# Optimization experiments

Measured on AMD Instinct MI355X. Metric: run time of the kernel, lower is better.

Reference implementation:

```python
import jax, jax.numpy as jnp
import numpy as np

N, E = 50000, 1600000
FEAT, HID, HEADS = 256, 64, 2
NEG_SLOPE = 0.2


def gat_conv(x, src, dst, W, att_src, att_dst, bias, heads, out_ch):
    """PyG GATConv (concat=True, self-loops already appended to src/dst)."""
    n = x.shape[0]
    h = (x @ W).reshape(n, heads, out_ch)                      # [N,H,C]
    a_src = jnp.einsum('nhc,hc->nh', h, att_src)               # [N,H]
    a_dst = jnp.einsum('nhc,hc->nh', h, att_dst)               # [N,H]
    alpha = jax.nn.leaky_relu(a_src[src] + a_dst[dst], NEG_SLOPE)  # [E',H]
    # segment softmax over incoming edges of each dst node
    amax = jax.ops.segment_max(alpha, dst, num_segments=n)
    alpha = jnp.exp(alpha - amax[dst])
    denom = jax.ops.segment_sum(alpha, dst, num_segments=n)
    alpha = alpha / (denom[dst] + 1e-16)
    msg = h[src] * alpha[..., None]                            # [E',H,C]
    out = jax.ops.segment_sum(msg, dst, num_segments=n)        # [N,H,C]
    return out.reshape(n, heads * out_ch) + bias


def setup_inputs() -> dict:
    key = jax.random.key(0)
    ks = jax.random.split(key, 10)
    x = jax.random.normal(ks[0], (N, FEAT), dtype=jnp.float32)
    edge_index = jax.random.randint(ks[1], (2, E), 0, N, dtype=jnp.int64)
    s1 = 1.0 / np.sqrt(FEAT)
    s2 = 1.0 / np.sqrt(HID * HEADS)
    sa = 1.0 / np.sqrt(HID)
    return {
        'x': x,
        'edge_index': edge_index,
        'W1': jax.random.uniform(ks[2], (FEAT, HEADS * HID), jnp.float32, -s1, s1),
        'att_src1': jax.random.uniform(ks[3], (HEADS, HID), jnp.float32, -sa, sa),
        'att_dst1': jax.random.uniform(ks[4], (HEADS, HID), jnp.float32, -sa, sa),
        'b1': jnp.zeros((HEADS * HID,), jnp.float32),
        'W2': jax.random.uniform(ks[5], (HEADS * HID, HID), jnp.float32, -s2, s2),
        'att_src2': jax.random.uniform(ks[6], (1, HID), jnp.float32, -sa, sa),
        'att_dst2': jax.random.uniform(ks[7], (1, HID), jnp.float32, -sa, sa),
        'b2': jnp.zeros((HID,), jnp.float32),
    }


def reference(x, edge_index, W1, att_src1, att_dst1, b1, W2, att_src2, att_dst2, b2):
    n = x.shape[0]
    loop = jnp.arange(n, dtype=edge_index.dtype)
    src = jnp.concatenate([edge_index[0], loop])   # add self loops (PyG default)
    dst = jnp.concatenate([edge_index[1], loop])
    h = gat_conv(x, src, dst, W1, att_src1, att_dst1, b1, HEADS, HID)
    h = jax.nn.relu(h)  # dropout is identity in eval mode
    h = gat_conv(h, src, dst, W2, att_src2, att_dst2, b2, 1, HID)
    return jax.nn.log_softmax(h, axis=1)
```

## Files before the change

kernel.cpp:

```cpp
#include <hip/hip_runtime.h>
#include <hip/hip_bf16.h>
#include <math.h>

typedef short bf16x8 __attribute__((ext_vector_type(8)));
typedef float f32x4 __attribute__((ext_vector_type(4)));

#define BSHIFT 7
#define BWIDTH 128
#define PCHUNK 4096


__global__ void zero_buf(int* __restrict__ p, int n) {
    int i = blockIdx.x * blockDim.x + threadIdx.x;
    if (i < n) p[i] = 0;
}

__global__ __launch_bounds__(256) void bucket_hist(const int* __restrict__ ei, int E,
                                                   int* __restrict__ bcnt) {
    __shared__ int h[512];
    int tid = threadIdx.x;
    for (int i = tid; i < 512; i += 256) h[i] = 0;
    __syncthreads();
    int start = blockIdx.x * PCHUNK;
    int cnt = min(PCHUNK, E - start);
    for (int i = tid; i < cnt; i += 256)
        atomicAdd(&h[ei[E + start + i] >> BSHIFT], 1);
    __syncthreads();
    for (int i = tid; i < 512; i += 256)
        if (h[i]) atomicAdd(&bcnt[i], h[i]);
}

__global__ __launch_bounds__(512) void bucket_scan(const int* __restrict__ bcnt,
                                                   int* __restrict__ bbase,
                                                   int* __restrict__ bcur,
                                                   int nbk, int n) {
    __shared__ int s[512];
    int tid = threadIdx.x;
    int nodes = 0;
    if (tid < nbk) nodes = min(BWIDTH, n - (tid << BSHIFT));
    int v = (tid < nbk) ? bcnt[tid] + nodes : 0;
    s[tid] = v;
    __syncthreads();
    #pragma unroll
    for (int o = 1; o < 512; o <<= 1) {
        int t = (tid >= o) ? s[tid - o] : 0;
        __syncthreads();
        s[tid] += t;
        __syncthreads();
    }
    if (tid < nbk) {
        int ex = s[tid] - v;
        bbase[tid] = ex;
        bcur[tid] = ex - (tid << BSHIFT);
    }
    if (tid == nbk) bbase[nbk] = s[tid];
}

__global__ __launch_bounds__(256) void partition_edges(const int* __restrict__ ei, int E,
                                                       int* __restrict__ bcur,
                                                       int* __restrict__ tmp) {
    __shared__ int2 stage[PCHUNK];
    __shared__ int h[512];
    __shared__ int lbase[512];
    int tid = threadIdx.x;
    int start = blockIdx.x * PCHUNK;
    int cnt = min(PCHUNK, E - start);
    for (int i = tid; i < 512; i += 256) h[i] = 0;
    __syncthreads();
    for (int i = tid; i < cnt; i += 256) {
        int s = ei[start + i];
        int d = ei[E + start + i];
        stage[i] = make_int2(s, d);
        atomicAdd(&h[d >> BSHIFT], 1);
    }
    __syncthreads();
    for (int i = tid; i < 512; i += 256) {
        if (h[i] > 0) lbase[i] = atomicAdd(&bcur[i], h[i]);
        h[i] = 0;
    }
    __syncthreads();
    for (int i = tid; i < cnt; i += 256) {
        int2 e = stage[i];
        int b = e.y >> BSHIFT;
        int r = atomicAdd(&h[b], 1);
        tmp[lbase[b] + r] = (e.x << BSHIFT) | (e.y & (BWIDTH - 1));
    }
}

__global__ __launch_bounds__(256) void bucket_csr(const int* __restrict__ bbase,
                                                  const int* __restrict__ tmp,
                                                  int* __restrict__ offs,
                                                  int* __restrict__ srcs,
                                                  int n, int nbk) {
    __shared__ int cnt[BWIDTH];
    __shared__ int sa[BWIDTH];
    __shared__ int cur[BWIDTH];
    int b = blockIdx.x;
    int tid = threadIdx.x;
    int node0 = b << BSHIFT;
    int nnodes = min(BWIDTH, n - node0);
    int cb = bbase[b];
    int ce = bbase[b + 1];
    int tb = cb - node0;
    int ecnt = (ce - cb) - nnodes;

    if (tid < BWIDTH) cnt[tid] = (tid < nnodes) ? 1 : 0;
    __syncthreads();
    for (int i = tid; i < ecnt; i += 256)
        atomicAdd(&cnt[tmp[tb + i] & (BWIDTH - 1)], 1);
    __syncthreads();
    if (tid < BWIDTH) sa[tid] = cnt[tid];
    __syncthreads();
    #pragma unroll
    for (int o = 1; o < BWIDTH; o <<= 1) {
        int v = 0;
        if (tid < BWIDTH) { v = sa[tid]; if (tid >= o) v += sa[tid - o]; }
        __syncthreads();
        if (tid < BWIDTH) sa[tid] = v;
        __syncthreads();
    }
    if (tid < BWIDTH) {
        int ex = sa[tid] - cnt[tid];
        if (tid < nnodes) {
            offs[node0 + tid] = cb + ex;
            srcs[cb + ex] = node0 + tid;
        }
        cur[tid] = ex + (tid < nnodes ? 1 : 0);
    }
    if (b == nbk - 1 && tid == 0) offs[n] = ce;
    __syncthreads();
    for (int i = tid; i < ecnt; i += 256) {
        int e = tmp[tb + i];
        int li = e & (BWIDTH - 1);
        int r = atomicAdd(&cur[li], 1);
        srcs[cb + r] = e >> BSHIFT;
    }
}

__global__ void transpose_both(const float* __restrict__ W1, const float* __restrict__ W2,
                               __hip_bfloat16* __restrict__ W1t,
                               __hip_bfloat16* __restrict__ W2t) {
    int idx = blockIdx.x * blockDim.x + threadIdx.x;
    const int n1 = 128 * 256;
    if (idx < n1) {
        int nn = idx >> 8, kk = idx & 255;
        W1t[idx] = __float2bfloat16(W1[kk * 128 + nn]);
    } else {
        int j = idx - n1;
        if (j < 64 * 128) {
            int nn = j >> 7, kk = j & 127;
            W2t[j] = __float2bfloat16(W2[kk * 64 + nn]);
        }
    }
}

template <bool A_BF16, int NT, int HEADS>
__global__ __launch_bounds__(256) void gemm_att(
    const void* __restrict__ Av, const __hip_bfloat16* __restrict__ Bt,
    __hip_bfloat16* __restrict__ C,
    const float* __restrict__ atts, const float* __restrict__ attd,
    float* __restrict__ a_s, float* __restrict__ a_d, int M, int K) {
    constexpr int N = NT * 16;
    __shared__ __hip_bfloat16 As[64][40];
    int tid = threadIdx.x;
    int w = tid >> 6, l = tid & 63;
    int q = l >> 4, m16 = l & 15;
    int bm = blockIdx.x * 64;

    int lr = tid >> 2, lseg = tid & 3;
    int arow = bm + lr; if (arow >= M) arow = M - 1;

    f32x4 acc[NT];
    #pragma unroll
    for (int t = 0; t < NT; t++) acc[t] = (f32x4){0.f, 0.f, 0.f, 0.f};

    for (int kc = 0; kc < K; kc += 32) {
        if (A_BF16) {
            const __hip_bfloat16* A = (const __hip_bfloat16*)Av;
            uint4 v = *(const uint4*)(A + (size_t)arow * K + kc + lseg * 8);
            *(uint4*)&As[lr][lseg * 8] = v;
        } else {
            const float* A = (const float*)Av;
            float4 v0 = *(const float4*)(A + (size_t)arow * K + kc + lseg * 8);
            float4 v1 = *(const float4*)(A + (size_t)arow * K + kc + lseg * 8 + 4);
            union { __hip_bfloat16 h[8]; uint4 u; } tmp;
            tmp.h[0] = __float2bfloat16(v0.x); tmp.h[1] = __float2bfloat16(v0.y);
            tmp.h[2] = __float2bfloat16(v0.z); tmp.h[3] = __float2bfloat16(v0.w);
            tmp.h[4] = __float2bfloat16(v1.x); tmp.h[5] = __float2bfloat16(v1.y);
            tmp.h[6] = __float2bfloat16(v1.z); tmp.h[7] = __float2bfloat16(v1.w);
            *(uint4*)&As[lr][lseg * 8] = tmp.u;
        }
        __syncthreads();
        bf16x8 a = *(const bf16x8*)&As[w * 16 + m16][q * 8];
        #pragma unroll
        for (int t = 0; t < NT; t++) {
            bf16x8 b = *(const bf16x8*)(Bt + (size_t)(t * 16 + m16) * K + kc + q * 8);
            acc[t] = __builtin_amdgcn_mfma_f32_16x16x32_bf16(a, b, acc[t], 0, 0, 0);
        }
        __syncthreads();
    }

    #pragma unroll
    for (int t = 0; t < NT; t++) {
        #pragma unroll
        for (int r = 0; r < 4; r++) {
            int row = bm + w * 16 + q * 4 + r;
            if (row < M) C[(size_t)row * N + t * 16 + m16] = __float2bfloat16(acc[t][r]);
        }
    }

    float ps[HEADS][4], pd[HEADS][4];
    #pragma unroll
    for (int hh = 0; hh < HEADS; hh++)
        #pragma unroll
        for (int r = 0; r < 4; r++) { ps[hh][r] = 0.f; pd[hh][r] = 0.f; }
    #pragma unroll
    for (int t = 0; t < NT; t++) {
        int ch = t * 16 + m16;
        float asw = atts[ch], adw = attd[ch];
        int hh = (HEADS == 2) ? (t >> 2) : 0;
        #pragma unroll
        for (int r = 0; r < 4; r++) {
            ps[hh][r] = fmaf(acc[t][r], asw, ps[hh][r]);
            pd[hh][r] = fmaf(acc[t][r], adw, pd[hh][r]);
        }
    }
    #pragma unroll
    for (int o = 1; o < 16; o <<= 1) {
        #pragma unroll
        for (int hh = 0; hh < HEADS; hh++)
            #pragma unroll
            for (int r = 0; r < 4; r++) {
                ps[hh][r] += __shfl_xor(ps[hh][r], o);
                pd[hh][r] += __shfl_xor(pd[hh][r], o);
            }
    }
    if (m16 == 0) {
        #pragma unroll
        for (int r = 0; r < 4; r++) {
            int row = bm + w * 16 + q * 4 + r;
            if (row < M) {
                if (HEADS == 2) {
                    a_s[row * 2]     = ps[0][r];
                    a_s[row * 2 + 1] = ps[1][r];
                    a_d[row * 2]     = pd[0][r];
                    a_d[row * 2 + 1] = pd[1][r];
                } else {
                    a_s[row] = ps[0][r];
                    a_d[row] = pd[0][r];
                }
            }
        }
    }
}

__device__ __forceinline__ float leaky(float r) {
    return r < 0.f ? 0.2f * r : r;
}

__device__ __forceinline__ void unpack2(unsigned u, float& lo, float& hi) {
    lo = __uint_as_float(u << 16);
    hi = __uint_as_float(u & 0xffff0000u);
}

__global__ __launch_bounds__(256) void edge_agg_l1(
    const int* __restrict__ offs, const int* __restrict__ srcs,
    const __hip_bfloat16* __restrict__ h1, const float* __restrict__ asv,
    const float* __restrict__ adv, const float* __restrict__ bias,
    __hip_bfloat16* __restrict__ out, int n) {
    int wid = (blockIdx.x * blockDim.x + threadIdx.x) >> 6;
    int lane = threadIdx.x & 63;
    int d = wid >> 1;
    int h = wid & 1;
    if (d >= n) return;
    int start = offs[d], end = offs[d + 1];
    float adh = adv[2 * d + h];

    float m = -3.4e38f, ssum = 0.f;
    for (int e = start + lane; e < end; e += 64) {
        int s = srcs[e];
        float r = leaky(asv[2 * s + h] + adh);
        if (r > m) { ssum *= __expf(m - r); m = r; }
        ssum += __expf(r - m);
    }
    #pragma unroll
    for (int o = 1; o < 64; o <<= 1) {
        float om = __shfl_xor(m, o), os = __shfl_xor(ssum, o);
        float nm = fmaxf(m, om);
        ssum = ssum * __expf(m - nm) + os * __expf(om - nm);
        m = nm;
    }
    float inv = 1.f / (ssum + 1e-16f);

    int sub = lane & 7;
    int g = lane >> 3;
    int ch0 = h * 64 + sub * 8;

    float acc[8];
    #pragma unroll
    for (int k = 0; k < 8; k++) acc[k] = 0.f;

    for (int base = start; base < end; base += 64) {
        int cnt = min(64, end - base);
        int s_l = 0;
        float w_l = 0.f;
        if (lane < cnt) {
            s_l = srcs[base + lane];
            w_l = __expf(leaky(asv[2 * s_l + h] + adh) - m) * inv;
        }
        int steps = (cnt + 7) >> 3;
        for (int jj = 0; jj < steps; ++jj) {
            int e = jj * 8 + g;
            float we = __shfl(w_l, e);
            int se = __shfl(s_l, e);
            uint4 v = *(const uint4*)(h1 + (size_t)se * 128 + ch0);
            float f0, f1, f2, f3, f4, f5, f6, f7;
            unpack2(v.x, f0, f1);
            unpack2(v.y, f2, f3);
            unpack2(v.z, f4, f5);
            unpack2(v.w, f6, f7);
            acc[0] = fmaf(we, f0, acc[0]);
            acc[1] = fmaf(we, f1, acc[1]);
            acc[2] = fmaf(we, f2, acc[2]);
            acc[3] = fmaf(we, f3, acc[3]);
            acc[4] = fmaf(we, f4, acc[4]);
            acc[5] = fmaf(we, f5, acc[5]);
            acc[6] = fmaf(we, f6, acc[6]);
            acc[7] = fmaf(we, f7, acc[7]);
        }
    }
    #pragma unroll
    for (int o = 8; o < 64; o <<= 1)
        #pragma unroll
        for (int k = 0; k < 8; k++) acc[k] += __shfl_xor(acc[k], o);

    if (lane < 8) {
        float4 b0 = *(const float4*)(bias + ch0);
        float4 b1 = *(const float4*)(bias + ch0 + 4);
        union { __hip_bfloat16 h[8]; uint4 u; } o2;
        o2.h[0] = __float2bfloat16(fmaxf(acc[0] + b0.x, 0.f));
        o2.h[1] = __float2bfloat16(fmaxf(acc[1] + b0.y, 0.f));
        o2.h[2] = __float2bfloat16(fmaxf(acc[2] + b0.z, 0.f));
        o2.h[3] = __float2bfloat16(fmaxf(acc[3] + b0.w, 0.f));
        o2.h[4] = __float2bfloat16(fmaxf(acc[4] + b1.x, 0.f));
        o2.h[5] = __float2bfloat16(fmaxf(acc[5] + b1.y, 0.f));
        o2.h[6] = __float2bfloat16(fmaxf(acc[6] + b1.z, 0.f));
        o2.h[7] = __float2bfloat16(fmaxf(acc[7] + b1.w, 0.f));
        *(uint4*)(out + (size_t)d * 128 + ch0) = o2.u;
    }
}

__global__ __launch_bounds__(256) void edge_agg_l2(
    const int* __restrict__ offs, const int* __restrict__ srcs,
    const __hip_bfloat16* __restrict__ h2, const float* __restrict__ asv,
    const float* __restrict__ adv, const float* __restrict__ bias,
    float* __restrict__ out, int n) {
    int d = (blockIdx.x * blockDim.x + threadIdx.x) >> 6;
    int lane = threadIdx.x & 63;
    if (d >= n) return;
    int start = offs[d], end = offs[d + 1];
    float ad = adv[d];

    float m = -3.4e38f, ssum = 0.f;
    for (int e = start + lane; e < end; e += 64) {
        int s = srcs[e];
        float r = leaky(asv[s] + ad);
        if (r > m) { ssum *= __expf(m - r); m = r; }
        ssum += __expf(r - m);
    }
    #pragma unroll
    for (int o = 1; o < 64; o <<= 1) {
        float om = __shfl_xor(m, o), os = __shfl_xor(ssum, o);
        float nm = fmaxf(m, om);
        ssum = ssum * __expf(m - nm) + os * __expf(om - nm);
        m = nm;
    }
    float inv = 1.f / (ssum + 1e-16f);

    int sub = lane & 7;
    int g = lane >> 3;
    int ch0 = sub * 8;

    float acc[8];
    #pragma unroll
    for (int k = 0; k < 8; k++) acc[k] = 0.f;

    for (int base = start; base < end; base += 64) {
        int cnt = min(64, end - base);
        int s_l = 0;
        float w_l = 0.f;
        if (lane < cnt) {
            s_l = srcs[base + lane];
            w_l = __expf(leaky(asv[s_l] + ad) - m) * inv;
        }
        int steps = (cnt + 7) >> 3;
        for (int jj = 0; jj < steps; ++jj) {
            int e = jj * 8 + g;
            float we = __shfl(w_l, e);
            int se = __shfl(s_l, e);
            uint4 v = *(const uint4*)(h2 + (size_t)se * 64 + ch0);
            float f0, f1, f2, f3, f4, f5, f6, f7;
            unpack2(v.x, f0, f1);
            unpack2(v.y, f2, f3);
            unpack2(v.z, f4, f5);
            unpack2(v.w, f6, f7);
            acc[0] = fmaf(we, f0, acc[0]);
            acc[1] = fmaf(we, f1, acc[1]);
            acc[2] = fmaf(we, f2, acc[2]);
            acc[3] = fmaf(we, f3, acc[3]);
            acc[4] = fmaf(we, f4, acc[4]);
            acc[5] = fmaf(we, f5, acc[5]);
            acc[6] = fmaf(we, f6, acc[6]);
            acc[7] = fmaf(we, f7, acc[7]);
        }
    }
    #pragma unroll
    for (int o = 8; o < 64; o <<= 1)
        #pragma unroll
        for (int k = 0; k < 8; k++) acc[k] += __shfl_xor(acc[k], o);

    float4 b0 = *(const float4*)(bias + ch0);
    float4 b1 = *(const float4*)(bias + ch0 + 4);
    float v[8];
    v[0] = acc[0] + b0.x; v[1] = acc[1] + b0.y;
    v[2] = acc[2] + b0.z; v[3] = acc[3] + b0.w;
    v[4] = acc[4] + b1.x; v[5] = acc[5] + b1.y;
    v[6] = acc[6] + b1.z; v[7] = acc[7] + b1.w;

    float vm = v[0];
    #pragma unroll
    for (int k = 1; k < 8; k++) vm = fmaxf(vm, v[k]);
    #pragma unroll
    for (int o = 1; o < 8; o <<= 1) vm = fmaxf(vm, __shfl_xor(vm, o));
    float se_loc = 0.f;
    #pragma unroll
    for (int k = 0; k < 8; k++) se_loc += __expf(v[k] - vm);
    #pragma unroll
    for (int o = 1; o < 8; o <<= 1) se_loc += __shfl_xor(se_loc, o);
    float lse = vm + logf(se_loc);

    if (lane < 8) {
        float4 o0 = make_float4(v[0] - lse, v[1] - lse, v[2] - lse, v[3] - lse);
        float4 o1 = make_float4(v[4] - lse, v[5] - lse, v[6] - lse, v[7] - lse);
        *(float4*)(out + (size_t)d * 64 + ch0) = o0;
        *(float4*)(out + (size_t)d * 64 + ch0 + 4) = o1;
    }
}

extern "C" void kernel_launch(void* const* d_in, const int* in_sizes, int n_in,
                              void* d_out, int out_size, void* d_ws, size_t ws_size,
                              hipStream_t stream) {
    const float* x    = (const float*)d_in[0];
    const int*   ei   = (const int*)d_in[1];
    const float* W1   = (const float*)d_in[2];
    const float* as1w = (const float*)d_in[3];
    const float* ad1w = (const float*)d_in[4];
    const float* b1   = (const float*)d_in[5];
    const float* W2   = (const float*)d_in[6];
    const float* as2w = (const float*)d_in[7];
    const float* ad2w = (const float*)d_in[8];
    const float* b2   = (const float*)d_in[9];
    float* out = (float*)d_out;

    const int n = in_sizes[0] / 256;
    const int E = in_sizes[1] / 2;
    const int tot = E + n;
    const int nbk = (n + BWIDTH - 1) / BWIDTH;

    char* p = (char*)d_ws;
    auto alloc = [&](size_t bytes) {
        void* r = (void*)p;
        p += (bytes + 255) & ~(size_t)255;
        return r;
    };
    int*   offs  = (int*)alloc((size_t)(n + 1) * 4);
    int*   srcs  = (int*)alloc((size_t)tot * 4);
    int*   tmp   = (int*)alloc((size_t)E * 4);
    int*   bcnt  = (int*)alloc(512 * 4);
    int*   bbase = (int*)alloc(512 * 4);
    int*   bcur  = (int*)alloc(512 * 4);
    __hip_bfloat16* W1t = (__hip_bfloat16*)alloc((size_t)128 * 256 * 2);
    __hip_bfloat16* W2t = (__hip_bfloat16*)alloc((size_t)64 * 128 * 2);
    __hip_bfloat16* h1  = (__hip_bfloat16*)alloc((size_t)n * 128 * 2);
    __hip_bfloat16* out1= (__hip_bfloat16*)alloc((size_t)n * 128 * 2);
    __hip_bfloat16* h2  = (__hip_bfloat16*)alloc((size_t)n * 64 * 2);
    float* a_s1 = (float*)alloc((size_t)n * 2 * 4);
    float* a_d1 = (float*)alloc((size_t)n * 2 * 4);
    float* a_s2 = (float*)alloc((size_t)n * 4);
    float* a_d2 = (float*)alloc((size_t)n * 4);

    int pblocks = (E + PCHUNK - 1) / PCHUNK;

    zero_buf<<<2, 256, 0, stream>>>(bcnt, 512);
    bucket_hist<<<pblocks, 256, 0, stream>>>(ei, E, bcnt);
    bucket_scan<<<1, 512, 0, stream>>>(bcnt, bbase, bcur, nbk, n);
    partition_edges<<<pblocks, 256, 0, stream>>>(ei, E, bcur, tmp);
    bucket_csr<<<nbk, 256, 0, stream>>>(bbase, tmp, offs, srcs, n, nbk);

    transpose_both<<<(128 * 256 + 64 * 128 + 255) / 256, 256, 0, stream>>>(W1, W2, W1t, W2t);

    gemm_att<false, 8, 2><<<(n + 63) / 64, 256, 0, stream>>>(
        x, W1t, h1, as1w, ad1w, a_s1, a_d1, n, 256);
    edge_agg_l1<<<((size_t)n * 2 * 64 + 255) / 256, 256, 0, stream>>>(
        offs, srcs, h1, a_s1, a_d1, b1, out1, n);

    gemm_att<true, 4, 1><<<(n + 63) / 64, 256, 0, stream>>>(
        out1, W2t, h2, as2w, ad2w, a_s2, a_d2, n, 128);
    edge_agg_l2<<<((size_t)n * 64 + 255) / 256, 256, 0, stream>>>(
        offs, srcs, h2, a_s2, a_d2, b2, out, n);
}
```

Measured before the change: 319.4 us.

## Use single-pass online softmax in GAT edge aggregation and merge heads per wave

Both edge aggregation kernels now do the segment softmax in one pass. Each 64-edge chunk updates a running max and sum, rescales the accumulators when the max grows, and normalizes once at the end. This removes the separate first pass over srcs and the attention scores. Layer 1 now handles both heads in one wavefront (16 lanes across 128 channels, 4 edges in flight), which halves the wave count and reads both attention scores with one float2 load. The gather loops are unrolled by two to keep more loads in flight, at the cost of extra cross-lane reductions per chunk and more registers.

```diff
diff --git a/kernel.cpp b/kernel.cpp
--- a/kernel.cpp
+++ b/kernel.cpp
@@ -268,34 +268,18 @@
     const __hip_bfloat16* __restrict__ h1, const float* __restrict__ asv,
     const float* __restrict__ adv, const float* __restrict__ bias,
     __hip_bfloat16* __restrict__ out, int n) {
-    int wid = (blockIdx.x * blockDim.x + threadIdx.x) >> 6;
+    int d = (blockIdx.x * blockDim.x + threadIdx.x) >> 6;
     int lane = threadIdx.x & 63;
-    int d = wid >> 1;
-    int h = wid & 1;
     if (d >= n) return;
     int start = offs[d], end = offs[d + 1];
-    float adh = adv[2 * d + h];
-
-    float m = -3.4e38f, ssum = 0.f;
-    for (int e = start + lane; e < end; e += 64) {
-        int s = srcs[e];
-        float r = leaky(asv[2 * s + h] + adh);
-        if (r > m) { ssum *= __expf(m - r); m = r; }
-        ssum += __expf(r - m);
-    }
-    #pragma unroll
-    for (int o = 1; o < 64; o <<= 1) {
-        float om = __shfl_xor(m, o), os = __shfl_xor(ssum, o);
-        float nm = fmaxf(m, om);
-        ssum = ssum * __expf(m - nm) + os * __expf(om - nm);
-        m = nm;
-    }
-    float inv = 1.f / (ssum + 1e-16f);
-
-    int sub = lane & 7;
-    int g = lane >> 3;
-    int ch0 = h * 64 + sub * 8;
-
+    float ad0 = adv[2 * d], ad1 = adv[2 * d + 1];
+
+    int sub = lane & 15;
+    int g = lane >> 4;
+    int ch0 = sub * 8;
+    int hsel = sub >> 3;
+
+    float m0 = -3.4e38f, m1 = -3.4e38f, s0 = 0.f, s1 = 0.f;
     float acc[8];
     #pragma unroll
     for (int k = 0; k < 8; k++) acc[k] = 0.f;
@@ -303,49 +287,97 @@
     for (int base = start; base < end; base += 64) {
         int cnt = min(64, end - base);
         int s_l = 0;
-        float w_l = 0.f;
+        float r0 = -3.4e38f, r1 = -3.4e38f;
         if (lane < cnt) {
             s_l = srcs[base + lane];
-            w_l = __expf(leaky(asv[2 * s_l + h] + adh) - m) * inv;
-        }
-        int steps = (cnt + 7) >> 3;
-        for (int jj = 0; jj < steps; ++jj) {
-            int e = jj * 8 + g;
-            float we = __shfl(w_l, e);
-            int se = __shfl(s_l, e);
-            uint4 v = *(const uint4*)(h1 + (size_t)se * 128 + ch0);
+            float2 a = *(const float2*)(asv + 2 * s_l);
+            r0 = leaky(a.x + ad0);
+            r1 = leaky(a.y + ad1);
+        }
+        float bm0 = r0, bm1 = r1;
+        #pragma unroll
+        for (int o = 1; o < 64; o <<= 1) {
+            bm0 = fmaxf(bm0, __shfl_xor(bm0, o));
+            bm1 = fmaxf(bm1, __shfl_xor(bm1, o));
+        }
+        float nm0 = fmaxf(m0, bm0), nm1 = fmaxf(m1, bm1);
+        float sc0 = __expf(m0 - nm0), sc1 = __expf(m1 - nm1);
+        float e0 = __expf(r0 - nm0);
+        float e1 = __expf(r1 - nm1);
+        float bs0 = e0, bs1 = e1;
+        #pragma unroll
+        for (int o = 1; o < 64; o <<= 1) {
+            bs0 += __shfl_xor(bs0, o);
+            bs1 += __shfl_xor(bs1, o);
+        }
+        s0 = s0 * sc0 + bs0;
+        s1 = s1 * sc1 + bs1;
+        m0 = nm0; m1 = nm1;
+        if (sc0 < 1.f || sc1 < 1.f) {
+            float sch = hsel ? sc1 : sc0;
+            #pragma unroll
+            for (int k = 0; k < 8; k++) acc[k] *= sch;
+        }
+
+        int steps = (cnt + 3) >> 2;
+        int jj = 0;
+        for (; jj + 2 <= steps; jj += 2) {
+            int eA = jj * 4 + g, eB = eA + 4;
+            float w0A = __shfl(e0, eA), w1A = __shfl(e1, eA);
+            int sA = __shfl(s_l, eA);
+            float w0B = __shfl(e0, eB), w1B = __shfl(e1, eB);
+            int sB = __shfl(s_l, eB);
+            float wA = hsel ? w1A : w0A;
+            float wB = hsel ? w1B : w0B;
+            uint4 vA = *(const uint4*)(h1 + (size_t)sA * 128 + ch0);
+            uint4 vB = *(const uint4*)(h1 + (size_t)sB * 128 + ch0);
             float f0, f1, f2, f3, f4, f5, f6, f7;
-            unpack2(v.x, f0, f1);
-            unpack2(v.y, f2, f3);
-            unpack2(v.z, f4, f5);
-            unpack2(v.w, f6, f7);
-            acc[0] = fmaf(we, f0, acc[0]);
-            acc[1] = fmaf(we, f1, acc[1]);
-            acc[2] = fmaf(we, f2, acc[2]);
-            acc[3] = fmaf(we, f3, acc[3]);
-            acc[4] = fmaf(we, f4, acc[4]);
-            acc[5] = fmaf(we, f5, acc[5]);
-            acc[6] = fmaf(we, f6, acc[6]);
-            acc[7] = fmaf(we, f7, acc[7]);
-        }
-    }
-    #pragma unroll
-    for (int o = 8; o < 64; o <<= 1)
+            unpack2(vA.x, f0, f1); unpack2(vA.y, f2, f3);
+            unpack2(vA.z, f4, f5); unpack2(vA.w, f6, f7);
+            acc[0] = fmaf(wA, f0, acc[0]); acc[1] = fmaf(wA, f1, acc[1]);
+            acc[2] = fmaf(wA, f2, acc[2]); acc[3] = fmaf(wA, f3, acc[3]);
+            acc[4] = fmaf(wA, f4, acc[4]); acc[5] = fmaf(wA, f5, acc[5]);
+            acc[6] = fmaf(wA, f6, acc[6]); acc[7] = fmaf(wA, f7, acc[7]);
+            unpack2(vB.x, f0, f1); unpack2(vB.y, f2, f3);
+            unpack2(vB.z, f4, f5); unpack2(vB.w, f6, f7);
+            acc[0] = fmaf(wB, f0, acc[0]); acc[1] = fmaf(wB, f1, acc[1]);
+            acc[2] = fmaf(wB, f2, acc[2]); acc[3] = fmaf(wB, f3, acc[3]);
+            acc[4] = fmaf(wB, f4, acc[4]); acc[5] = fmaf(wB, f5, acc[5]);
+            acc[6] = fmaf(wB, f6, acc[6]); acc[7] = fmaf(wB, f7, acc[7]);
+        }
+        if (jj < steps) {
+            int eA = jj * 4 + g;
+            float w0A = __shfl(e0, eA), w1A = __shfl(e1, eA);
+            int sA = __shfl(s_l, eA);
+            float wA = hsel ? w1A : w0A;
+            uint4 vA = *(const uint4*)(h1 + (size_t)sA * 128 + ch0);
+            float f0, f1, f2, f3, f4, f5, f6, f7;
+            unpack2(vA.x, f0, f1); unpack2(vA.y, f2, f3);
+            unpack2(vA.z, f4, f5); unpack2(vA.w, f6, f7);
+            acc[0] = fmaf(wA, f0, acc[0]); acc[1] = fmaf(wA, f1, acc[1]);
+            acc[2] = fmaf(wA, f2, acc[2]); acc[3] = fmaf(wA, f3, acc[3]);
+            acc[4] = fmaf(wA, f4, acc[4]); acc[5] = fmaf(wA, f5, acc[5]);
+            acc[6] = fmaf(wA, f6, acc[6]); acc[7] = fmaf(wA, f7, acc[7]);
+        }
+    }
+    #pragma unroll
+    for (int o = 16; o < 64; o <<= 1)
         #pragma unroll
         for (int k = 0; k < 8; k++) acc[k] += __shfl_xor(acc[k], o);
 
-    if (lane < 8) {
+    if (lane < 16) {
+        float invh = 1.f / ((hsel ? s1 : s0) + 1e-16f);
         float4 b0 = *(const float4*)(bias + ch0);
         float4 b1 = *(const float4*)(bias + ch0 + 4);
         union { __hip_bfloat16 h[8]; uint4 u; } o2;
-        o2.h[0] = __float2bfloat16(fmaxf(acc[0] + b0.x, 0.f));
-        o2.h[1] = __float2bfloat16(fmaxf(acc[1] + b0.y, 0.f));
-        o2.h[2] = __float2bfloat16(fmaxf(acc[2] + b0.z, 0.f));
-        o2.h[3] = __float2bfloat16(fmaxf(acc[3] + b0.w, 0.f));
-        o2.h[4] = __float2bfloat16(fmaxf(acc[4] + b1.x, 0.f));
-        o2.h[5] = __float2bfloat16(fmaxf(acc[5] + b1.y, 0.f));
-        o2.h[6] = __float2bfloat16(fmaxf(acc[6] + b1.z, 0.f));
-        o2.h[7] = __float2bfloat16(fmaxf(acc[7] + b1.w, 0.f));
+        o2.h[0] = __float2bfloat16(fmaxf(fmaf(acc[0], invh, b0.x), 0.f));
+        o2.h[1] = __float2bfloat16(fmaxf(fmaf(acc[1], invh, b0.y), 0.f));
+        o2.h[2] = __float2bfloat16(fmaxf(fmaf(acc[2], invh, b0.z), 0.f));
+        o2.h[3] = __float2bfloat16(fmaxf(fmaf(acc[3], invh, b0.w), 0.f));
+        o2.h[4] = __float2bfloat16(fmaxf(fmaf(acc[4], invh, b1.x), 0.f));
+        o2.h[5] = __float2bfloat16(fmaxf(fmaf(acc[5], invh, b1.y), 0.f));
+        o2.h[6] = __float2bfloat16(fmaxf(fmaf(acc[6], invh, b1.z), 0.f));
+        o2.h[7] = __float2bfloat16(fmaxf(fmaf(acc[7], invh, b1.w), 0.f));
         *(uint4*)(out + (size_t)d * 128 + ch0) = o2.u;
     }
 }
@@ -361,26 +393,11 @@
     int start = offs[d], end = offs[d + 1];
     float ad = adv[d];
 
-    float m = -3.4e38f, ssum = 0.f;
-    for (int e = start + lane; e < end; e += 64) {
-        int s = srcs[e];
-        float r = leaky(asv[s] + ad);
-        if (r > m) { ssum *= __expf(m - r); m = r; }
-        ssum += __expf(r - m);
-    }
-    #pragma unroll
-    for (int o = 1; o < 64; o <<= 1) {
-        float om = __shfl_xor(m, o), os = __shfl_xor(ssum, o);
-        float nm = fmaxf(m, om);
-        ssum = ssum * __expf(m - nm) + os * __expf(om - nm);
-        m = nm;
-    }
-    float inv = 1.f / (ssum + 1e-16f);
-
     int sub = lane & 7;
     int g = lane >> 3;
     int ch0 = sub * 8;
 
+    float m = -3.4e38f, ssum = 0.f;
     float acc[8];
     #pragma unroll
     for (int k = 0; k < 8; k++) acc[k] = 0.f;
@@ -388,30 +405,63 @@
     for (int base = start; base < end; base += 64) {
         int cnt = min(64, end - base);
         int s_l = 0;
-        float w_l = 0.f;
+        float r = -3.4e38f;
         if (lane < cnt) {
             s_l = srcs[base + lane];
-            w_l = __expf(leaky(asv[s_l] + ad) - m) * inv;
-        }
+            r = leaky(asv[s_l] + ad);
+        }
+        float bm = r;
+        #pragma unroll
+        for (int o = 1; o < 64; o <<= 1) bm = fmaxf(bm, __shfl_xor(bm, o));
+        float nm = fmaxf(m, bm);
+        float sc = __expf(m - nm);
+        float ew = __expf(r - nm);
+        float bs = ew;
+        #pragma unroll
+        for (int o = 1; o < 64; o <<= 1) bs += __shfl_xor(bs, o);
+        ssum = ssum * sc + bs;
+        m = nm;
+        if (sc < 1.f) {
+            #pragma unroll
+            for (int k = 0; k < 8; k++) acc[k] *= sc;
+        }
+
         int steps = (cnt + 7) >> 3;
-        for (int jj = 0; jj < steps; ++jj) {
-            int e = jj * 8 + g;
-            float we = __shfl(w_l, e);
-            int se = __shfl(s_l, e);
-            uint4 v = *(const uint4*)(h2 + (size_t)se * 64 + ch0);
+        int jj = 0;
+        for (; jj + 2 <= steps; jj += 2) {
+            int eA = jj * 8 + g, eB = eA + 8;
+            float wA = __shfl(ew, eA);
+            int sA = __shfl(s_l, eA);
+            float wB = __shfl(ew, eB);
+            int sB = __shfl(s_l, eB);
+            uint4 vA = *(const uint4*)(h2 + (size_t)sA * 64 + ch0);
+            uint4 vB = *(const uint4*)(h2 + (size_t)sB * 64 + ch0);
             float f0, f1, f2, f3, f4, f5, f6, f7;
-            unpack2(v.x, f0, f1);
-            unpack2(v.y, f2, f3);
-            unpack2(v.z, f4, f5);
-            unpack2(v.w, f6, f7);
-            acc[0] = fmaf(we, f0, acc[0]);
-            acc[1] = fmaf(we, f1, acc[1]);
-            acc[2] = fmaf(we, f2, acc[2]);
-            acc[3] = fmaf(we, f3, acc[3]);
-            acc[4] = fmaf(we, f4, acc[4]);
-            acc[5] = fmaf(we, f5, acc[5]);
-            acc[6] = fmaf(we, f6, acc[6]);
-            acc[7] = fmaf(we, f7, acc[7]);
+            unpack2(vA.x, f0, f1); unpack2(vA.y, f2, f3);
+            unpack2(vA.z, f4, f5); unpack2(vA.w, f6, f7);
+            acc[0] = fmaf(wA, f0, acc[0]); acc[1] = fmaf(wA, f1, acc[1]);
+            acc[2] = fmaf(wA, f2, acc[2]); acc[3] = fmaf(wA, f3, acc[3]);
+            acc[4] = fmaf(wA, f4, acc[4]); acc[5] = fmaf(wA, f5, acc[5]);
+            acc[6] = fmaf(wA, f6, acc[6]); acc[7] = fmaf(wA, f7, acc[7]);
+            unpack2(vB.x, f0, f1); unpack2(vB.y, f2, f3);
+            unpack2(vB.z, f4, f5); unpack2(vB.w, f6, f7);
+            acc[0] = fmaf(wB, f0, acc[0]); acc[1] = fmaf(wB, f1, acc[1]);
+            acc[2] = fmaf(wB, f2, acc[2]); acc[3] = fmaf(wB, f3, acc[3]);
+            acc[4] = fmaf(wB, f4, acc[4]); acc[5] = fmaf(wB, f5, acc[5]);
+            acc[6] = fmaf(wB, f6, acc[6]); acc[7] = fmaf(wB, f7, acc[7]);
+        }
+        if (jj < steps) {
+            int eA = jj * 8 + g;
+            float wA = __shfl(ew, eA);
+            int sA = __shfl(s_l, eA);
+            uint4 vA = *(const uint4*)(h2 + (size_t)sA * 64 + ch0);
+            float f0, f1, f2, f3, f4, f5, f6, f7;
+            unpack2(vA.x, f0, f1); unpack2(vA.y, f2, f3);
+            unpack2(vA.z, f4, f5); unpack2(vA.w, f6, f7);
+            acc[0] = fmaf(wA, f0, acc[0]); acc[1] = fmaf(wA, f1, acc[1]);
+            acc[2] = fmaf(wA, f2, acc[2]); acc[3] = fmaf(wA, f3, acc[3]);
+            acc[4] = fmaf(wA, f4, acc[4]); acc[5] = fmaf(wA, f5, acc[5]);
+            acc[6] = fmaf(wA, f6, acc[6]); acc[7] = fmaf(wA, f7, acc[7]);
         }
     }
     #pragma unroll
@@ -419,13 +469,14 @@
         #pragma unroll
         for (int k = 0; k < 8; k++) acc[k] += __shfl_xor(acc[k], o);
 
+    float inv = 1.f / (ssum + 1e-16f);
     float4 b0 = *(const float4*)(bias + ch0);
     float4 b1 = *(const float4*)(bias + ch0 + 4);
     float v[8];
-    v[0] = acc[0] + b0.x; v[1] = acc[1] + b0.y;
-    v[2] = acc[2] + b0.z; v[3] = acc[3] + b0.w;
-    v[4] = acc[4] + b1.x; v[5] = acc[5] + b1.y;
-    v[6] = acc[6] + b1.z; v[7] = acc[7] + b1.w;
+    v[0] = fmaf(acc[0], inv, b0.x); v[1] = fmaf(acc[1], inv, b0.y);
+    v[2] = fmaf(acc[2], inv, b0.z); v[3] = fmaf(acc[3], inv, b0.w);
+    v[4] = fmaf(acc[4], inv, b1.x); v[5] = fmaf(acc[5], inv, b1.y);
+    v[6] = fmaf(acc[6], inv, b1.z); v[7] = fmaf(acc[7], inv, b1.w);
 
     float vm = v[0];
     #pragma unroll
@@ -501,7 +552,7 @@
 
     gemm_att<false, 8, 2><<<(n + 63) / 64, 256, 0, stream>>>(
         x, W1t, h1, as1w, ad1w, a_s1, a_d1, n, 256);
-    edge_agg_l1<<<((size_t)n * 2 * 64 + 255) / 256, 256, 0, stream>>>(
+    edge_agg_l1<<<((size_t)n * 64 + 255) / 256, 256, 0, stream>>>(
         offs, srcs, h1, a_s1, a_d1, b1, out1, n);
 
     gemm_att<true, 4, 1><<<(n + 63) / 64, 256, 0, stream>>>(
```

Result: faster. 295.3 us (-7.6%).
